# Optimization experiments

Measured on AMD Instinct MI355X. Metric: run time of the kernel, lower is better.

Reference implementation:

```python
import jax, jax.numpy as jnp
import numpy as np

H, D, J, T, IN = 8, 32, 22, 6, 256   # heads, head_dim, joint_num, time_len-2, input_dim
S = 3 * J                            # sequence axis of attention (66)
NEG = -9e15


def _domain_mask():
    m = np.ones((S, S), np.float32)
    m[0:J, 2 * J:3 * J] = 0.0
    m[2 * J:3 * J, 0:J] = 0.0
    return jnp.asarray(m)


def setup_inputs() -> dict:
    key = jax.random.key(0)
    ks = jax.random.split(key, 5)
    s = 0.02
    return {
        "x": jax.random.normal(ks[0], (512, T, S, IN), jnp.float32),
        "Wq": jax.random.normal(ks[1], (H * D, IN), jnp.float32) * s,
        "bq": jnp.zeros((H * D,), jnp.float32),
        "Wk": jax.random.normal(ks[2], (H * D, IN), jnp.float32) * s,
        "bk": jnp.zeros((H * D,), jnp.float32),
        "Wv": jax.random.normal(ks[3], (H * D, IN), jnp.float32) * s,
        "bv": jnp.zeros((H * D,), jnp.float32),
        "Wc": jax.random.normal(ks[4], (J, S), jnp.float32) * s,
        "bc": jnp.zeros((J,), jnp.float32),
    }


def reference(x, Wq, bq, Wk, bk, Wv, bv, Wc, bc):
    B = x.shape[0]
    mask = _domain_mask()

    def proj(W, b):
        # (B,T,S,IN) @ (IN,H*D) -> (B,T,S,H,D) -> (B,T,H,S,D)
        return (x @ W.T + b).reshape(B, T, S, H, D).transpose(0, 1, 3, 2, 4)

    q = proj(Wq, bq)
    k = proj(Wk, bk)
    v = jax.nn.relu(proj(Wv, bv))

    scores = jnp.einsum('bthqd,bthkd->bthqk', q, k) / jnp.sqrt(jnp.float32(D))
    scores = scores * mask
    # joint_num == 22 branch: threshold-based pruning against row max
    m = jnp.max(scores, axis=-1, keepdims=True)
    scores = jnp.where(jnp.abs(scores) <= m / 9.0, NEG, scores)
    attn = jax.nn.softmax(scores, axis=-1)

    out = jnp.einsum('bthqk,bthkd->bthqd', attn, v)          # (B,T,H,S,D)
    # cls Linear over the S axis: (B,T,H,D,S) -> (B,T,H,D,J), then back to (B,T,H,J,D)
    out = jnp.einsum('bthsd,js->bthjd', out, Wc) + bc[None, None, None, :, None]
    out = out.transpose(0, 1, 3, 2, 4)                        # (B,T,J,H,D)
    return out.reshape(B, T * J, H * D)
```

## Files before the change

### kernel.cpp

```cpp
#include <hip/hip_runtime.h>
#include <hip/hip_bf16.h>


constexpr int T  = 6;
constexpr int S  = 66;
constexpr int IN = 256;
constexpr int H  = 8;
constexpr int D  = 32;
constexpr int J  = 22;
constexpr float NEG = -9e15f;
constexpr float INV_SQRT_D = 0.17677669529663688110f;

#define XM2H_OFF 16384
#define XM2L_OFF 20480
#define W_OFF    24576
#define W_LO     12288
#define QH_OFF   0
#define QL_OFF   4752
#define KH_OFF   9504
#define KL_OFF   14256
#define VTH_OFF  27456
#define VTL_OFF  34112
#define INV_OFF  40768
#define AOT_OFF  41040
#define PH_OFF   0
#define PL_OFF   13728
#define WCH_OFF  27456
#define WCL_OFF  34112
#define SMEM_BYTES 49152

#define WSW_STRIDE 24576
#define WSWC_OFF   786432
#define WS_W       799744ull
#define XIMG_OFF   799744
#define XIMG_BT    65536
#define WS_FULL    (799744ull + 3072ull * 65536ull)

typedef float f32x4   __attribute__((ext_vector_type(4)));
typedef float f32x16  __attribute__((ext_vector_type(16)));
typedef short bf16x8  __attribute__((ext_vector_type(8)));
typedef short s4v     __attribute__((ext_vector_type(4)));

__device__ __forceinline__ unsigned cvtpk(float a, float b) {
    unsigned r;
    asm("v_cvt_pk_bf16_f32 %0, %1, %2" : "=v"(r) : "v"(a), "v"(b));
    return r;
}
__device__ __forceinline__ float bfh2f(unsigned short h) {
    return __uint_as_float(((unsigned)h) << 16);
}
__device__ __forceinline__ void split2(float a, float b, unsigned& hi, unsigned& lo) {
    unsigned h = cvtpk(a, b);
    float ra = a - __uint_as_float(h << 16);
    float rb = b - __uint_as_float(h & 0xffff0000u);
    lo = cvtpk(ra, rb);
    hi = h;
}
__device__ __forceinline__ bf16x8 ld_bf16x8_a8(const short* p) {
    s4v a = *(const s4v*)p;
    s4v b = *(const s4v*)(p + 4);
    return __builtin_shufflevector(a, b, 0, 1, 2, 3, 4, 5, 6, 7);
}
__device__ __forceinline__ void gload16(const void* g, void* l) {
    __builtin_amdgcn_global_load_lds(
        (const __attribute__((address_space(1))) unsigned*)g,
        (__attribute__((address_space(3))) unsigned*)l, 16, 0, 0);
}

__global__ __launch_bounds__(256)
void presplit_kernel(const float* __restrict__ Wq, const float* __restrict__ Wk,
                     const float* __restrict__ Wv, const float* __restrict__ Wc,
                     unsigned char* __restrict__ ws)
{
    int gid = blockIdx.x * 256 + threadIdx.x;
    if (gid < 49152) {
        int img = gid / 1536, u = gid - img * 1536;
        int row = u >> 4, c = u & 15, k0 = c << 2;
        int mat = row >> 5, dd = row & 31;
        int chunk = img & 3, hh = img >> 2;
        const float* Wm = (mat == 0) ? Wq : (mat == 1) ? Wk : Wv;
        float4 v = *(const float4*)(Wm + (size_t)(hh * 32 + dd) * IN + chunk * 64 + c * 4);
        uint2 hi, lo;
        split2(v.x, v.y, hi.x, lo.x);
        split2(v.z, v.w, hi.y, lo.y);
        int tile  = (mat << 2) + (k0 >> 4);
        int lanei = dd + (((k0 >> 3) & 1) << 5);
        int byte  = (tile << 10) + (lanei << 4) + ((k0 & 7) << 1);
        unsigned char* base = ws + (size_t)img * WSW_STRIDE;
        *(uint2*)(base + byte)        = hi;
        *(uint2*)(base + W_LO + byte) = lo;
    } else if (gid < 49152 + 1664) {
        int g2  = gid - 49152;
        int row = g2 / 52, cu = g2 - row * 52;
        int c0  = 2 * cu;
        float a = (row < 22 && c0     < 66) ? Wc[row * 66 + c0]     : 0.f;
        float b = (row < 22 && c0 + 1 < 66) ? Wc[row * 66 + c0 + 1] : 0.f;
        unsigned hi, lo;
        split2(a, b, hi, lo);
        *(unsigned*)(ws + WSWC_OFF + row * 208 + 4 * cu)        = hi;
        *(unsigned*)(ws + WSWC_OFF + 6656 + row * 208 + 4 * cu) = lo;
    }
}

__global__ __launch_bounds__(256)
void presplit_x_kernel(const float* __restrict__ x, unsigned char* __restrict__ ws)
{
    __shared__ __align__(16) unsigned char lds[16384];
    const int tid = threadIdx.x;
    const int chunk = blockIdx.x & 3;
    const int bt = blockIdx.x >> 2;
    const float* xg = x + (size_t)bt * S * IN + chunk * 64;
    for (int u = tid; u < 1024; u += 256) {
        int s = u >> 4, c = u & 15;
        int rel = ((s << 7) + (c << 3)) ^ ((s & 7) << 4);
        float4 v = *(const float4*)(xg + (size_t)s * IN + c * 4);
        uint2 hi, lo;
        split2(v.x, v.y, hi.x, lo.x);
        split2(v.z, v.w, hi.y, lo.y);
        *(uint2*)(lds + rel)        = hi;
        *(uint2*)(lds + 8192 + rel) = lo;
    }
    __syncthreads();
    const int lane = tid & 63, wid = tid >> 6;
    unsigned char* img = ws + XIMG_OFF + (size_t)bt * XIMG_BT + chunk * 16384;
    for (int i = wid; i < 16; i += 4) {
        int comp = (i >= 8) ? 1 : 0;
        int ti = i - comp * 8;
        int mtile = ti >> 2, ks = ti & 3;
        int row = mtile * 32 + (lane & 31);
        int rel = ((row << 7) + (ks << 5) + ((lane >> 5) << 4)) ^ ((row & 7) << 4);
        uint4 v = *(const uint4*)(lds + comp * 8192 + rel);
        *(uint4*)(img + (i << 10) + (lane << 4)) = v;
    }
}

template<int MODE>
__global__ __launch_bounds__(256, 3)
void mha_fused_kernel(const float* __restrict__ x,
                      const float* __restrict__ Wq, const float* __restrict__ bq,
                      const float* __restrict__ Wk, const float* __restrict__ bk,
                      const float* __restrict__ Wv, const float* __restrict__ bv,
                      const float* __restrict__ Wc, const float* __restrict__ bc,
                      const unsigned char* __restrict__ ws,
                      float* __restrict__ out)
{
    __shared__ __align__(16) unsigned char smem[SMEM_BYTES];

    const int tid = threadIdx.x;
    const int i0  = blockIdx.x;
    const int h   = (i0 >> 3) & 7;
    const int bt  = (i0 & 7) | ((i0 >> 6) << 3);

    const int wid  = tid >> 6;
    const int lane = tid & 63;
    const int l15  = lane & 15;
    const int quad = lane >> 4;

    for (int u = tid; u < 512; u += 256)
        *(uint4*)(smem + XM2H_OFF + u * 16) = (uint4){0u, 0u, 0u, 0u};

    const f32x16 zacc = {0.f,0.f,0.f,0.f,0.f,0.f,0.f,0.f,0.f,0.f,0.f,0.f,0.f,0.f,0.f,0.f};
    f32x16 accs[3] = {zacc, zacc, zacc};

    const float* xg0 = x + (size_t)bt * S * IN;
    for (int chunk = 0; chunk < 4; ++chunk) {
        __syncthreads();
        const float* xg = xg0 + chunk * 64;
        if constexpr (MODE == 2) {
            const unsigned char* ximg = ws + XIMG_OFF + (size_t)bt * XIMG_BT + chunk * 16384;
            const unsigned char* wimg = ws + (size_t)((h << 2) | chunk) * WSW_STRIDE;
            for (int i = wid; i < 16; i += 4)
                gload16(ximg + (i << 10) + (lane << 4), smem + (i << 10));
            for (int i = wid; i < 24; i += 4)
                gload16(wimg + (i << 10) + (lane << 4), smem + W_OFF + (i << 10));
            if (tid < 32) {
                int s = 64 + (tid >> 4), c = tid & 15;
                float4 v = *(const float4*)(xg + (size_t)s * IN + c * 4);
                uint2 hi, lo;
                split2(v.x, v.y, hi.x, lo.x);
                split2(v.z, v.w, hi.y, lo.y);
                int off = ((c >> 2) << 10) + (((s & 31) + (((c >> 1) & 1) << 5)) << 4)
                        + ((c & 1) << 3);
                *(uint2*)(smem + XM2H_OFF + off) = hi;
                *(uint2*)(smem + XM2L_OFF + off) = lo;
            }
        } else {
            if constexpr (MODE == 1) {
                const unsigned char* wimg = ws + (size_t)((h << 2) | chunk) * WSW_STRIDE;
                for (int i = wid; i < 24; i += 4)
                    gload16(wimg + (i << 10) + (lane << 4), smem + W_OFF + (i << 10));
            } else {
                for (int u = tid; u < 1536; u += 256) {
                    int row = u >> 4, c = u & 15, k0 = c << 2;
                    int mat = row >> 5, dd2 = row & 31;
                    const float* Wm = (mat == 0) ? Wq : (mat == 1) ? Wk : Wv;
                    float4 v = *(const float4*)(Wm + (size_t)(h * 32 + dd2) * IN + chunk * 64 + c * 4);
                    uint2 hi, lo;
                    split2(v.x, v.y, hi.x, lo.x);
                    split2(v.z, v.w, hi.y, lo.y);
                    int tile  = (mat << 2) + (k0 >> 4);
                    int lanei = dd2 + (((k0 >> 3) & 1) << 5);
                    int byte  = (tile << 10) + (lanei << 4) + ((k0 & 7) << 1);
                    *(uint2*)(smem + W_OFF + byte)        = hi;
                    *(uint2*)(smem + W_OFF + W_LO + byte) = lo;
                }
            }
            for (int u = tid; u < 1536; u += 256) {
                int s = u >> 4, c = u & 15, k0 = c << 2;
                uint2 hi = {0u, 0u}, lo = {0u, 0u};
                if (s < 66) {
                    float4 v = *(const float4*)(xg + (size_t)s * IN + c * 4);
                    split2(v.x, v.y, hi.x, lo.x);
                    split2(v.z, v.w, hi.y, lo.y);
                }
                int ks = k0 >> 4, khalf = (k0 >> 3) & 1, b = (k0 & 7) << 1;
                int off = (ks << 10) + (((s & 31) + (khalf << 5)) << 4) + b;
                if (s < 64) {
                    int base = (s >> 5) * 4096 + off;
                    *(uint2*)(smem + base)        = hi;
                    *(uint2*)(smem + base + 8192) = lo;
                } else {
                    *(uint2*)(smem + XM2H_OFF + off) = hi;
                    *(uint2*)(smem + XM2L_OFF + off) = lo;
                }
            }
        }
        __syncthreads();

        #pragma unroll
        for (int t = 0; t < 3; ++t) {
            int p = wid + 4 * t;
            if (p >= 9) break;
            int mtile = p / 3, mat = p - mtile * 3;
            const unsigned char *xaH, *xaL;
            if (mtile < 2) { xaH = smem + ((mtile * 4) << 10) + (lane << 4); xaL = xaH + 8192; }
            else           { xaH = smem + XM2H_OFF + (lane << 4);            xaL = xaH + 4096; }
            const unsigned char* wbH = smem + W_OFF + ((mat * 4) << 10) + (lane << 4);
            #pragma unroll
            for (int ks = 0; ks < 4; ++ks) {
                bf16x8 ah = *(const bf16x8*)(xaH + (ks << 10));
                bf16x8 al = *(const bf16x8*)(xaL + (ks << 10));
                bf16x8 bh = *(const bf16x8*)(wbH + (ks << 10));
                bf16x8 bl = *(const bf16x8*)(wbH + (ks << 10) + W_LO);
                accs[t] = __builtin_amdgcn_mfma_f32_32x32x16_bf16(ah, bh, accs[t], 0, 0, 0);
                accs[t] = __builtin_amdgcn_mfma_f32_32x32x16_bf16(ah, bl, accs[t], 0, 0, 0);
                accs[t] = __builtin_amdgcn_mfma_f32_32x32x16_bf16(al, bh, accs[t], 0, 0, 0);
            }
        }
    }
    __syncthreads();

    {
        short* qh = (short*)(smem + QH_OFF); short* ql = (short*)(smem + QL_OFF);
        short* kh = (short*)(smem + KH_OFF); short* kl = (short*)(smem + KL_OFF);
        const int dd = lane & 31;
        const int half = lane >> 5;
        #pragma unroll
        for (int t = 0; t < 3; ++t) {
            int p = wid + 4 * t;
            if (p >= 9) break;
            int mtile = p / 3, mat = p - mtile * 3;
            const float* bias_p = (mat == 0) ? bq : (mat == 1) ? bk : bv;
            float bias = bias_p[h * 32 + dd];
            if (mat < 2) {
                short* bh_ = (mat == 0) ? qh : kh;
                short* bl_ = (mat == 0) ? ql : kl;
                #pragma unroll
                for (int g = 0; g < 4; ++g) {
                    int sb2 = mtile * 32 + half * 4 + 8 * g;
                    uint2 hi, lo;
                    split2(accs[t][4*g+0] + bias, accs[t][4*g+1] + bias, hi.x, lo.x);
                    split2(accs[t][4*g+2] + bias, accs[t][4*g+3] + bias, hi.y, lo.y);
                    unsigned hs[4] = { hi.x & 0xffffu, hi.x >> 16, hi.y & 0xffffu, hi.y >> 16 };
                    unsigned ls[4] = { lo.x & 0xffffu, lo.x >> 16, lo.y & 0xffffu, lo.y >> 16 };
                    #pragma unroll
                    for (int r = 0; r < 4; ++r) {
                        int s = sb2 + r;
                        if (s < 66) {
                            bh_[s * 36 + dd] = (short)hs[r];
                            bl_[s * 36 + dd] = (short)ls[r];
                        }
                    }
                }
            } else {
                #pragma unroll
                for (int g = 0; g < 4; ++g) {
                    int sb2 = mtile * 32 + half * 4 + 8 * g;
                    float vv[4];
                    #pragma unroll
                    for (int r = 0; r < 4; ++r) {
                        int s = sb2 + r;
                        vv[r] = (s < 66) ? fmaxf(accs[t][4*g+r] + bias, 0.f) : 0.f;
                    }
                    uint2 ph, pl;
                    split2(vv[0], vv[1], ph.x, pl.x);
                    split2(vv[2], vv[3], ph.y, pl.y);
                    *(uint2*)(smem + VTH_OFF + dd * 208 + 2 * sb2) = ph;
                    *(uint2*)(smem + VTL_OFF + dd * 208 + 2 * sb2) = pl;
                }
            }
        }
    }
    __syncthreads();

    {
        const short* qh = (const short*)(smem + QH_OFF);
        const short* ql = (const short*)(smem + QL_OFF);
        const short* kh = (const short*)(smem + KH_OFF);
        const short* kl = (const short*)(smem + KL_OFF);

        auto qk_mfma = [&](int mq, f32x4* acc) {
            int aoff = (mq * 16 + l15) * 36 + quad * 8;
            bf16x8 ah = ld_bf16x8_a8(qh + aoff);
            bf16x8 al = ld_bf16x8_a8(ql + aoff);
            #pragma unroll
            for (int mk = 0; mk < 5; ++mk) {
                int boff = (mk * 16 + l15) * 36 + quad * 8;
                bf16x8 bh = ld_bf16x8_a8(kh + boff);
                bf16x8 bl = ld_bf16x8_a8(kl + boff);
                f32x4 a = (f32x4){0.f, 0.f, 0.f, 0.f};
                a = __builtin_amdgcn_mfma_f32_16x16x32_bf16(ah, bh, a, 0, 0, 0);
                a = __builtin_amdgcn_mfma_f32_16x16x32_bf16(ah, bl, a, 0, 0, 0);
                a = __builtin_amdgcn_mfma_f32_16x16x32_bf16(al, bh, a, 0, 0, 0);
                acc[mk] = a;
            }
        };

        f32x4 accA[5], accB[5];
        qk_mfma(wid, accA);
        if (wid == 3) qk_mfma(4, accB);
        __syncthreads();

        short* Ph = (short*)(smem + PH_OFF);
        short* Pl = (short*)(smem + PL_OFF);
        float* inv = (float*)(smem + INV_OFF);

        auto sm_store = [&](int mq, f32x4* acc) {
            float v[5][4];
            #pragma unroll
            for (int mk = 0; mk < 5; ++mk) {
                int ks = mk * 16 + l15;
                #pragma unroll
                for (int reg = 0; reg < 4; ++reg) {
                    int qs = mq * 16 + quad * 4 + reg;
                    bool invalid = (qs >= 66) || (ks >= 66);
                    bool masked = (qs < J && ks >= 2 * J) || (qs >= 2 * J && ks < J);
                    float s = acc[mk][reg] * INV_SQRT_D;
                    v[mk][reg] = invalid ? -INFINITY : (masked ? 0.f : s);
                }
            }
            float rmax[4];
            #pragma unroll
            for (int reg = 0; reg < 4; ++reg) {
                float mm = fmaxf(fmaxf(fmaxf(v[0][reg], v[1][reg]),
                                       fmaxf(v[2][reg], v[3][reg])), v[4][reg]);
                mm = fmaxf(mm, __shfl_xor(mm, 1));
                mm = fmaxf(mm, __shfl_xor(mm, 2));
                mm = fmaxf(mm, __shfl_xor(mm, 4));
                mm = fmaxf(mm, __shfl_xor(mm, 8));
                const float thr = mm / 9.0f;
                float rm = -INFINITY;
                #pragma unroll
                for (int mk = 0; mk < 5; ++mk) {
                    float sv = v[mk][reg];
                    float pr = (fabsf(sv) <= thr) ? NEG : sv;
                    v[mk][reg] = pr;
                    rm = fmaxf(rm, pr);
                }
                rm = fmaxf(rm, __shfl_xor(rm, 1));
                rm = fmaxf(rm, __shfl_xor(rm, 2));
                rm = fmaxf(rm, __shfl_xor(rm, 4));
                rm = fmaxf(rm, __shfl_xor(rm, 8));
                rmax[reg] = rm;
            }
            #pragma unroll
            for (int reg = 0; reg < 4; ++reg) {
                int qs = mq * 16 + quad * 4 + reg;
                float e[5], lsum = 0.f;
                #pragma unroll
                for (int mk = 0; mk < 5; ++mk) {
                    float ev = __expf(v[mk][reg] - rmax[reg]);
                    e[mk] = ev;
                    lsum += ev;
                }
                lsum += __shfl_xor(lsum, 1);
                lsum += __shfl_xor(lsum, 2);
                lsum += __shfl_xor(lsum, 4);
                lsum += __shfl_xor(lsum, 8);
                if (qs < 66) {
                    #pragma unroll
                    for (int mk = 0; mk < 5; ++mk) {
                        int ks = mk * 16 + l15;
                        unsigned short hi = (unsigned short)cvtpk(e[mk], e[mk]);
                        unsigned short lo = (unsigned short)cvtpk(e[mk] - bfh2f(hi), 0.f);
                        Ph[qs * 104 + ks] = (short)hi;
                        Pl[qs * 104 + ks] = (short)lo;
                    }
                    if (l15 == 0) inv[qs] = 1.0f / lsum;
                }
            }
        };

        sm_store(wid, accA);
        if (wid == 3) sm_store(4, accB);

        for (int u = tid; u < 264; u += 256) {
            int comp = u >= 132 ? 1 : 0, rem = u - comp * 132;
            int row = rem >> 1, part = rem & 1;
            *(uint4*)(smem + (comp ? PL_OFF : PH_OFF) + row * 208 + 160 + part * 16)
                = (uint4){0u, 0u, 0u, 0u};
        }
    }
    __syncthreads();

    {
        const short* Ph = (const short*)(smem + PH_OFF);
        const short* Pl = (const short*)(smem + PL_OFF);
        const short* vh = (const short*)(smem + VTH_OFF);
        const short* vl = (const short*)(smem + VTL_OFF);
        const float* inv = (const float*)(smem + INV_OFF);
        for (int t = 0; t < 3; ++t) {
            int tt = wid + 4 * t;
            if (tt >= 10) break;
            int mq = tt >> 1, nd = tt & 1;
            f32x4 acc = (f32x4){0.f, 0.f, 0.f, 0.f};
            #pragma unroll
            for (int ks = 0; ks < 3; ++ks) {
                bf16x8 a   = *(const bf16x8*)(Ph + (mq * 16 + l15) * 104 + ks * 32 + quad * 8);
                bf16x8 al8 = *(const bf16x8*)(Pl + (mq * 16 + l15) * 104 + ks * 32 + quad * 8);
                bf16x8 b   = *(const bf16x8*)(vh + (nd * 16 + l15) * 104 + ks * 32 + quad * 8);
                bf16x8 bl8 = *(const bf16x8*)(vl + (nd * 16 + l15) * 104 + ks * 32 + quad * 8);
                acc = __builtin_amdgcn_mfma_f32_16x16x32_bf16(a, b, acc, 0, 0, 0);
                acc = __builtin_amdgcn_mfma_f32_16x16x32_bf16(al8, b, acc, 0, 0, 0);
                acc = __builtin_amdgcn_mfma_f32_16x16x32_bf16(a, bl8, acc, 0, 0, 0);
            }
            int dd = nd * 16 + l15, sbase = mq * 16 + quad * 4;
            float o[4];
            #pragma unroll
            for (int reg = 0; reg < 4; ++reg) {
                int qs = sbase + reg;
                o[reg] = (qs < 66) ? acc[reg] * inv[qs] : 0.f;
            }
            uint2 pk;
            pk.x = cvtpk(o[0], o[1]);
            pk.y = cvtpk(o[2], o[3]);
            *(uint2*)(smem + AOT_OFF + dd * 208 + 2 * sbase) = pk;
        }
        for (int u = tid; u < 384; u += 256) {
            int row = u / 12, kcol = 80 + 2 * (u % 12);
            *(unsigned*)(smem + AOT_OFF + row * 208 + 2 * kcol) = 0u;
        }
    }
    __syncthreads();

    if constexpr (MODE >= 1) {
        const unsigned char* wc = ws + WSWC_OFF;
        for (int i = wid; i < 13; i += 4)
            gload16(wc + (i << 10) + (lane << 4), smem + WCH_OFF + (i << 10));
    } else {
        for (int u = tid; u < 726; u += 256) {
            int row = u / 33, cp = u - row * 33;
            float2 w = *(const float2*)(Wc + row * 66 + 2 * cp);
            unsigned hi, lo;
            split2(w.x, w.y, hi, lo);
            *(unsigned*)(smem + WCH_OFF + row * 208 + 4 * cp) = hi;
            *(unsigned*)(smem + WCL_OFF + row * 208 + 4 * cp) = lo;
        }
        for (int u = tid; u < 836; u += 256) {
            int comp = u >= 418 ? 1 : 0, rem = comp ? u - 418 : u;
            int row = rem / 19, kcol = 66 + 2 * (rem % 19);
            *(unsigned*)(smem + (comp ? WCL_OFF : WCH_OFF) + row * 208 + 2 * kcol) = 0u;
        }
    }
    __syncthreads();

    {
        const short* Wch = (const short*)(smem + WCH_OFF);
        const short* Wcl = (const short*)(smem + WCL_OFF);
        const short* aoT = (const short*)(smem + AOT_OFF);
        int mj = wid >> 1, nd = wid & 1;
        f32x4 acc = (f32x4){0.f, 0.f, 0.f, 0.f};
        #pragma unroll
        for (int ks = 0; ks < 3; ++ks) {
            bf16x8 a   = *(const bf16x8*)(Wch + (mj * 16 + l15) * 104 + ks * 32 + quad * 8);
            bf16x8 al8 = *(const bf16x8*)(Wcl + (mj * 16 + l15) * 104 + ks * 32 + quad * 8);
            bf16x8 b   = *(const bf16x8*)(aoT + (nd * 16 + l15) * 104 + ks * 32 + quad * 8);
            acc = __builtin_amdgcn_mfma_f32_16x16x32_bf16(a, b, acc, 0, 0, 0);
            acc = __builtin_amdgcn_mfma_f32_16x16x32_bf16(al8, b, acc, 0, 0, 0);
        }
        int dd = nd * 16 + l15;
        #pragma unroll
        for (int reg = 0; reg < 4; ++reg) {
            int j = mj * 16 + quad * 4 + reg;
            if (j < 22) {
                size_t o = (size_t)(bt * J + j) * (H * D) + h * 32 + dd;
                out[o] = acc[reg] + bc[j];
            }
        }
    }
}

extern "C" void kernel_launch(void* const* d_in, const int* in_sizes, int n_in,
                              void* d_out, int out_size, void* d_ws, size_t ws_size,
                              hipStream_t stream) {
    const float* x  = (const float*)d_in[0];
    const float* Wq = (const float*)d_in[1];
    const float* bq = (const float*)d_in[2];
    const float* Wk = (const float*)d_in[3];
    const float* bk = (const float*)d_in[4];
    const float* Wv = (const float*)d_in[5];
    const float* bv = (const float*)d_in[6];
    const float* Wc = (const float*)d_in[7];
    const float* bc = (const float*)d_in[8];
    float* out = (float*)d_out;

    const int B = 512;
    dim3 grid(B * T * H), block(256);
    if (d_ws != nullptr && ws_size >= WS_FULL) {
        hipLaunchKernelGGL(presplit_kernel, dim3(199), dim3(256), 0, stream,
                           Wq, Wk, Wv, Wc, (unsigned char*)d_ws);
        hipLaunchKernelGGL(presplit_x_kernel, dim3(12288), dim3(256), 0, stream,
                           x, (unsigned char*)d_ws);
        hipLaunchKernelGGL((mha_fused_kernel<2>), grid, block, 0, stream,
                           x, Wq, bq, Wk, bk, Wv, bv, Wc, bc,
                           (const unsigned char*)d_ws, out);
    } else if (d_ws != nullptr && ws_size >= WS_W) {
        hipLaunchKernelGGL(presplit_kernel, dim3(199), dim3(256), 0, stream,
                           Wq, Wk, Wv, Wc, (unsigned char*)d_ws);
        hipLaunchKernelGGL((mha_fused_kernel<1>), grid, block, 0, stream,
                           x, Wq, bq, Wk, bk, Wv, bv, Wc, bc,
                           (const unsigned char*)d_ws, out);
    } else {
        hipLaunchKernelGGL((mha_fused_kernel<0>), grid, block, 0, stream,
                           x, Wq, bq, Wk, bk, Wv, bv, Wc, bc,
                           (const unsigned char*)nullptr, out);
    }
}
```

Baseline: 942.9 us.

## Drop x presplit pass and transpose QK^T so softmax rows span lanes

Removes the separate presplit_x kernel and the MODE 2 path, which wrote a bf16 hi/lo image of x to workspace. Each block now converts x from fp32 in-kernel, which avoids an extra full round trip of x through global memory. QK^T is also transposed: keys become the MFMA A operand, so each lane holds one query row across registers. Row max and sum then need only two cross-lane shuffles per row instead of four per register, and P is written with packed 8-byte stores. In exchange every head-block re-reads and re-splits x itself, which is redundant across the 8 heads.

```diff
diff --git a/kernel.cpp b/kernel.cpp
--- a/kernel.cpp
+++ b/kernel.cpp
@@ -32,9 +32,6 @@
 #define WSW_STRIDE 24576
 #define WSWC_OFF   786432
 #define WS_W       799744ull
-#define XIMG_OFF   799744
-#define XIMG_BT    65536
-#define WS_FULL    (799744ull + 3072ull * 65536ull)
 
 typedef float f32x4   __attribute__((ext_vector_type(4)));
 typedef float f32x16  __attribute__((ext_vector_type(16)));
@@ -102,38 +99,6 @@
     }
 }
 
-__global__ __launch_bounds__(256)
-void presplit_x_kernel(const float* __restrict__ x, unsigned char* __restrict__ ws)
-{
-    __shared__ __align__(16) unsigned char lds[16384];
-    const int tid = threadIdx.x;
-    const int chunk = blockIdx.x & 3;
-    const int bt = blockIdx.x >> 2;
-    const float* xg = x + (size_t)bt * S * IN + chunk * 64;
-    for (int u = tid; u < 1024; u += 256) {
-        int s = u >> 4, c = u & 15;
-        int rel = ((s << 7) + (c << 3)) ^ ((s & 7) << 4);
-        float4 v = *(const float4*)(xg + (size_t)s * IN + c * 4);
-        uint2 hi, lo;
-        split2(v.x, v.y, hi.x, lo.x);
-        split2(v.z, v.w, hi.y, lo.y);
-        *(uint2*)(lds + rel)        = hi;
-        *(uint2*)(lds + 8192 + rel) = lo;
-    }
-    __syncthreads();
-    const int lane = tid & 63, wid = tid >> 6;
-    unsigned char* img = ws + XIMG_OFF + (size_t)bt * XIMG_BT + chunk * 16384;
-    for (int i = wid; i < 16; i += 4) {
-        int comp = (i >= 8) ? 1 : 0;
-        int ti = i - comp * 8;
-        int mtile = ti >> 2, ks = ti & 3;
-        int row = mtile * 32 + (lane & 31);
-        int rel = ((row << 7) + (ks << 5) + ((lane >> 5) << 4)) ^ ((row & 7) << 4);
-        uint4 v = *(const uint4*)(lds + comp * 8192 + rel);
-        *(uint4*)(img + (i << 10) + (lane << 4)) = v;
-    }
-}
-
 template<int MODE>
 __global__ __launch_bounds__(256, 3)
 void mha_fused_kernel(const float* __restrict__ x,
@@ -166,63 +131,42 @@
     for (int chunk = 0; chunk < 4; ++chunk) {
         __syncthreads();
         const float* xg = xg0 + chunk * 64;
-        if constexpr (MODE == 2) {
-            const unsigned char* ximg = ws + XIMG_OFF + (size_t)bt * XIMG_BT + chunk * 16384;
+        if constexpr (MODE == 1) {
             const unsigned char* wimg = ws + (size_t)((h << 2) | chunk) * WSW_STRIDE;
-            for (int i = wid; i < 16; i += 4)
-                gload16(ximg + (i << 10) + (lane << 4), smem + (i << 10));
             for (int i = wid; i < 24; i += 4)
                 gload16(wimg + (i << 10) + (lane << 4), smem + W_OFF + (i << 10));
-            if (tid < 32) {
-                int s = 64 + (tid >> 4), c = tid & 15;
-                float4 v = *(const float4*)(xg + (size_t)s * IN + c * 4);
+        } else {
+            for (int u = tid; u < 1536; u += 256) {
+                int row = u >> 4, c = u & 15, k0 = c << 2;
+                int mat = row >> 5, dd2 = row & 31;
+                const float* Wm = (mat == 0) ? Wq : (mat == 1) ? Wk : Wv;
+                float4 v = *(const float4*)(Wm + (size_t)(h * 32 + dd2) * IN + chunk * 64 + c * 4);
                 uint2 hi, lo;
                 split2(v.x, v.y, hi.x, lo.x);
                 split2(v.z, v.w, hi.y, lo.y);
-                int off = ((c >> 2) << 10) + (((s & 31) + (((c >> 1) & 1) << 5)) << 4)
-                        + ((c & 1) << 3);
+                int tile  = (mat << 2) + (k0 >> 4);
+                int lanei = dd2 + (((k0 >> 3) & 1) << 5);
+                int byte  = (tile << 10) + (lanei << 4) + ((k0 & 7) << 1);
+                *(uint2*)(smem + W_OFF + byte)        = hi;
+                *(uint2*)(smem + W_OFF + W_LO + byte) = lo;
+            }
+        }
+        for (int u = tid; u < 1536; u += 256) {
+            int s = u >> 4, c = u & 15, k0 = c << 2;
+            if (s >= 66) continue;
+            float4 v = *(const float4*)(xg + (size_t)s * IN + c * 4);
+            uint2 hi, lo;
+            split2(v.x, v.y, hi.x, lo.x);
+            split2(v.z, v.w, hi.y, lo.y);
+            int ks = k0 >> 4, khalf = (k0 >> 3) & 1, b = (k0 & 7) << 1;
+            int off = (ks << 10) + (((s & 31) + (khalf << 5)) << 4) + b;
+            if (s < 64) {
+                int base = (s >> 5) * 4096 + off;
+                *(uint2*)(smem + base)        = hi;
+                *(uint2*)(smem + base + 8192) = lo;
+            } else {
                 *(uint2*)(smem + XM2H_OFF + off) = hi;
                 *(uint2*)(smem + XM2L_OFF + off) = lo;
-            }
-        } else {
-            if constexpr (MODE == 1) {
-                const unsigned char* wimg = ws + (size_t)((h << 2) | chunk) * WSW_STRIDE;
-                for (int i = wid; i < 24; i += 4)
-                    gload16(wimg + (i << 10) + (lane << 4), smem + W_OFF + (i << 10));
-            } else {
-                for (int u = tid; u < 1536; u += 256) {
-                    int row = u >> 4, c = u & 15, k0 = c << 2;
-                    int mat = row >> 5, dd2 = row & 31;
-                    const float* Wm = (mat == 0) ? Wq : (mat == 1) ? Wk : Wv;
-                    float4 v = *(const float4*)(Wm + (size_t)(h * 32 + dd2) * IN + chunk * 64 + c * 4);
-                    uint2 hi, lo;
-                    split2(v.x, v.y, hi.x, lo.x);
-                    split2(v.z, v.w, hi.y, lo.y);
-                    int tile  = (mat << 2) + (k0 >> 4);
-                    int lanei = dd2 + (((k0 >> 3) & 1) << 5);
-                    int byte  = (tile << 10) + (lanei << 4) + ((k0 & 7) << 1);
-                    *(uint2*)(smem + W_OFF + byte)        = hi;
-                    *(uint2*)(smem + W_OFF + W_LO + byte) = lo;
-                }
-            }
-            for (int u = tid; u < 1536; u += 256) {
-                int s = u >> 4, c = u & 15, k0 = c << 2;
-                uint2 hi = {0u, 0u}, lo = {0u, 0u};
-                if (s < 66) {
-                    float4 v = *(const float4*)(xg + (size_t)s * IN + c * 4);
-                    split2(v.x, v.y, hi.x, lo.x);
-                    split2(v.z, v.w, hi.y, lo.y);
-                }
-                int ks = k0 >> 4, khalf = (k0 >> 3) & 1, b = (k0 & 7) << 1;
-                int off = (ks << 10) + (((s & 31) + (khalf << 5)) << 4) + b;
-                if (s < 64) {
-                    int base = (s >> 5) * 4096 + off;
-                    *(uint2*)(smem + base)        = hi;
-                    *(uint2*)(smem + base + 8192) = lo;
-                } else {
-                    *(uint2*)(smem + XM2H_OFF + off) = hi;
-                    *(uint2*)(smem + XM2L_OFF + off) = lo;
-                }
             }
         }
         __syncthreads();
@@ -310,14 +254,14 @@
         const short* kl = (const short*)(smem + KL_OFF);
 
         auto qk_mfma = [&](int mq, f32x4* acc) {
-            int aoff = (mq * 16 + l15) * 36 + quad * 8;
-            bf16x8 ah = ld_bf16x8_a8(qh + aoff);
-            bf16x8 al = ld_bf16x8_a8(ql + aoff);
+            int boff = (mq * 16 + l15) * 36 + quad * 8;
+            bf16x8 bh = ld_bf16x8_a8(qh + boff);
+            bf16x8 bl = ld_bf16x8_a8(ql + boff);
             #pragma unroll
             for (int mk = 0; mk < 5; ++mk) {
-                int boff = (mk * 16 + l15) * 36 + quad * 8;
-                bf16x8 bh = ld_bf16x8_a8(kh + boff);
-                bf16x8 bl = ld_bf16x8_a8(kl + boff);
+                int aoff = (mk * 16 + l15) * 36 + quad * 8;
+                bf16x8 ah = ld_bf16x8_a8(kh + aoff);
+                bf16x8 al = ld_bf16x8_a8(kl + aoff);
                 f32x4 a = (f32x4){0.f, 0.f, 0.f, 0.f};
                 a = __builtin_amdgcn_mfma_f32_16x16x32_bf16(ah, bh, a, 0, 0, 0);
                 a = __builtin_amdgcn_mfma_f32_16x16x32_bf16(ah, bl, a, 0, 0, 0);
@@ -336,68 +280,67 @@
         float* inv = (float*)(smem + INV_OFF);
 
         auto sm_store = [&](int mq, f32x4* acc) {
+            const int q = mq * 16 + l15;
             float v[5][4];
             #pragma unroll
             for (int mk = 0; mk < 5; ++mk) {
-                int ks = mk * 16 + l15;
                 #pragma unroll
                 for (int reg = 0; reg < 4; ++reg) {
-                    int qs = mq * 16 + quad * 4 + reg;
-                    bool invalid = (qs >= 66) || (ks >= 66);
-                    bool masked = (qs < J && ks >= 2 * J) || (qs >= 2 * J && ks < J);
+                    int k = mk * 16 + quad * 4 + reg;
+                    bool invalid = (k >= 66);
+                    bool masked = (q < J && k >= 2 * J) || (q >= 2 * J && k < J);
                     float s = acc[mk][reg] * INV_SQRT_D;
                     v[mk][reg] = invalid ? -INFINITY : (masked ? 0.f : s);
                 }
             }
-            float rmax[4];
-            #pragma unroll
-            for (int reg = 0; reg < 4; ++reg) {
-                float mm = fmaxf(fmaxf(fmaxf(v[0][reg], v[1][reg]),
-                                       fmaxf(v[2][reg], v[3][reg])), v[4][reg]);
-                mm = fmaxf(mm, __shfl_xor(mm, 1));
-                mm = fmaxf(mm, __shfl_xor(mm, 2));
-                mm = fmaxf(mm, __shfl_xor(mm, 4));
-                mm = fmaxf(mm, __shfl_xor(mm, 8));
-                const float thr = mm / 9.0f;
-                float rm = -INFINITY;
-                #pragma unroll
-                for (int mk = 0; mk < 5; ++mk) {
+            float mm = -INFINITY;
+            #pragma unroll
+            for (int mk = 0; mk < 5; ++mk)
+                #pragma unroll
+                for (int reg = 0; reg < 4; ++reg) mm = fmaxf(mm, v[mk][reg]);
+            mm = fmaxf(mm, __shfl_xor(mm, 16));
+            mm = fmaxf(mm, __shfl_xor(mm, 32));
+            const float thr = mm / 9.0f;
+            float rm = -INFINITY;
+            #pragma unroll
+            for (int mk = 0; mk < 5; ++mk) {
+                #pragma unroll
+                for (int reg = 0; reg < 4; ++reg) {
                     float sv = v[mk][reg];
                     float pr = (fabsf(sv) <= thr) ? NEG : sv;
                     v[mk][reg] = pr;
                     rm = fmaxf(rm, pr);
                 }
-                rm = fmaxf(rm, __shfl_xor(rm, 1));
-                rm = fmaxf(rm, __shfl_xor(rm, 2));
-                rm = fmaxf(rm, __shfl_xor(rm, 4));
-                rm = fmaxf(rm, __shfl_xor(rm, 8));
-                rmax[reg] = rm;
-            }
-            #pragma unroll
-            for (int reg = 0; reg < 4; ++reg) {
-                int qs = mq * 16 + quad * 4 + reg;
-                float e[5], lsum = 0.f;
+            }
+            rm = fmaxf(rm, __shfl_xor(rm, 16));
+            rm = fmaxf(rm, __shfl_xor(rm, 32));
+            float e[5][4], lsum = 0.f;
+            #pragma unroll
+            for (int mk = 0; mk < 5; ++mk) {
+                #pragma unroll
+                for (int reg = 0; reg < 4; ++reg) {
+                    float ev = __expf(v[mk][reg] - rm);
+                    e[mk][reg] = ev;
+                    lsum += ev;
+                }
+            }
+            lsum += __shfl_xor(lsum, 16);
+            lsum += __shfl_xor(lsum, 32);
+            if (q < 66) {
                 #pragma unroll
                 for (int mk = 0; mk < 5; ++mk) {
-                    float ev = __expf(v[mk][reg] - rmax[reg]);
-                    e[mk] = ev;
-                    lsum += ev;
-                }
-                lsum += __shfl_xor(lsum, 1);
-                lsum += __shfl_xor(lsum, 2);
-                lsum += __shfl_xor(lsum, 4);
-                lsum += __shfl_xor(lsum, 8);
-                if (qs < 66) {
-                    #pragma unroll
-                    for (int mk = 0; mk < 5; ++mk) {
-                        int ks = mk * 16 + l15;
-                        unsigned short hi = (unsigned short)cvtpk(e[mk], e[mk]);
-                        unsigned short lo = (unsigned short)cvtpk(e[mk] - bfh2f(hi), 0.f);
-                        Ph[qs * 104 + ks] = (short)hi;
-                        Pl[qs * 104 + ks] = (short)lo;
-                    }
-                    if (l15 == 0) inv[qs] = 1.0f / lsum;
-                }
+                    unsigned h0 = cvtpk(e[mk][0], e[mk][1]);
+                    unsigned h1 = cvtpk(e[mk][2], e[mk][3]);
+                    uint2 hi = {h0, h1}, lo;
+                    lo.x = cvtpk(e[mk][0] - bfh2f((unsigned short)h0),
+                                 e[mk][1] - bfh2f((unsigned short)(h0 >> 16)));
+                    lo.y = cvtpk(e[mk][2] - bfh2f((unsigned short)h1),
+                                 e[mk][3] - bfh2f((unsigned short)(h1 >> 16)));
+                    int kb = (mk * 16 + quad * 4) * 2;
+                    *(uint2*)((unsigned char*)Ph + q * 208 + kb) = hi;
+                    *(uint2*)((unsigned char*)Pl + q * 208 + kb) = lo;
+                }
+                if (quad == 0) inv[q] = 1.0f / lsum;
             }
         };
 
@@ -516,15 +459,7 @@
 
     const int B = 512;
     dim3 grid(B * T * H), block(256);
-    if (d_ws != nullptr && ws_size >= WS_FULL) {
-        hipLaunchKernelGGL(presplit_kernel, dim3(199), dim3(256), 0, stream,
-                           Wq, Wk, Wv, Wc, (unsigned char*)d_ws);
-        hipLaunchKernelGGL(presplit_x_kernel, dim3(12288), dim3(256), 0, stream,
-                           x, (unsigned char*)d_ws);
-        hipLaunchKernelGGL((mha_fused_kernel<2>), grid, block, 0, stream,
-                           x, Wq, bq, Wk, bk, Wv, bv, Wc, bc,
-                           (const unsigned char*)d_ws, out);
-    } else if (d_ws != nullptr && ws_size >= WS_W) {
+    if (d_ws != nullptr && ws_size >= WS_W) {
         hipLaunchKernelGGL(presplit_kernel, dim3(199), dim3(256), 0, stream,
                            Wq, Wk, Wv, Wc, (unsigned char*)d_ws);
         hipLaunchKernelGGL((mha_fused_kernel<1>), grid, block, 0, stream,
```

Measured after the change: 1.037 ms. 1.1x slower.
